# Performance work log

Measured on AMD Instinct MI355X. Metric: run time of the kernel, lower is better.

Reference implementation:

```python
import jax, jax.numpy as jnp
import numpy as np

N, HR, HEADS = 1024, 2048, 4
C1 = HR // HEADS                      # 512 per-head dim, conv1
H2 = 2 * HEADS                        # 8 heads, conv2
C2 = (2 * HR) // (2 * HEADS)          # 512 per-head dim, conv2
EPS = 1e-5


def setup_inputs() -> dict:
    key = jax.random.key(0)
    ks = jax.random.split(key, 20)
    s1 = 1.0 / np.sqrt(N)
    s2 = 1.0 / np.sqrt(HR)
    f32 = jnp.float32
    d = {"x": jax.random.normal(ks[0], (N, N), f32)}
    # conv1 params (in=N, out=HR)
    d["q1_w"] = jax.random.normal(ks[1], (N, HR), f32) * s1
    d["q1_b"] = jnp.zeros((HR,), f32)
    d["k1_w"] = jax.random.normal(ks[2], (N, HR), f32) * s1
    d["k1_b"] = jnp.zeros((HR,), f32)
    d["v1_w"] = jax.random.normal(ks[3], (N, HR), f32) * s1
    d["v1_b"] = jnp.zeros((HR,), f32)
    d["e1_w"] = jax.random.normal(ks[4], (HR,), f32) * 0.1   # lin_edge (edge_dim=1, no bias)
    d["s1_w"] = jax.random.normal(ks[5], (N, HR), f32) * s1  # lin_skip
    d["s1_b"] = jnp.zeros((HR,), f32)
    d["gn1_gamma"] = jnp.ones((HR,), f32)
    d["gn1_beta"] = jnp.zeros((HR,), f32)
    d["gn1_ms"] = jnp.ones((HR,), f32)
    # conv2 params (in=HR, out=2*HR)
    d["q2_w"] = jax.random.normal(ks[6], (HR, 2 * HR), f32) * s2
    d["q2_b"] = jnp.zeros((2 * HR,), f32)
    d["k2_w"] = jax.random.normal(ks[7], (HR, 2 * HR), f32) * s2
    d["k2_b"] = jnp.zeros((2 * HR,), f32)
    d["v2_w"] = jax.random.normal(ks[8], (HR, 2 * HR), f32) * s2
    d["v2_b"] = jnp.zeros((2 * HR,), f32)
    d["e2_w"] = jax.random.normal(ks[9], (2 * HR,), f32) * 0.1
    d["s2_w"] = jax.random.normal(ks[10], (HR, 2 * HR), f32) * s2
    d["s2_b"] = jnp.zeros((2 * HR,), f32)
    d["gn2_gamma"] = jnp.ones((2 * HR,), f32)
    d["gn2_beta"] = jnp.zeros((2 * HR,), f32)
    d["gn2_ms"] = jnp.ones((2 * HR,), f32)
    return d


def _tconv(x, A, qw, qb, kw, kb, vw, vb, ew, sw, sb, H, Cd):
    # TransformerConv over fully-connected meshgrid graph; edge (r -> c) carries scalar A[r, c].
    # key_j/value_j get +A[r,c]*We; the edge term factors out so no [N,N,H,C] tensor is built.
    n = x.shape[0]
    q = (x @ qw + qb).reshape(n, H, Cd)   # targets c
    k = (x @ kw + kb).reshape(n, H, Cd)   # sources r
    v = (x @ vw + vb).reshape(n, H, Cd)
    We = ew.reshape(H, Cd)
    qk = jnp.einsum('chd,rhd->crh', q, k)                 # [N_tgt, N_src, H]
    qe = jnp.einsum('chd,hd->ch', q, We)                  # q_c . We per head
    logits = (qk + A.T[:, :, None] * qe[:, None, :]) / jnp.sqrt(jnp.float32(Cd))
    alpha = jax.nn.softmax(logits, axis=1)                # softmax over sources per target
    out = jnp.einsum('crh,rhd->chd', alpha, v)
    out = out + jnp.einsum('crh,rc->ch', alpha, A)[:, :, None] * We[None]
    return out.reshape(n, H * Cd) + x @ sw + sb           # root/skip connection


def _gnorm(x, gamma, beta, ms):
    # GraphNorm over a single graph: learnable mean-scale, per-feature stats across nodes.
    mu = x.mean(axis=0)
    out = x - ms * mu
    var = (out * out).mean(axis=0)
    return gamma * out * jax.lax.rsqrt(var + EPS) + beta


def reference(x, q1_w, q1_b, k1_w, k1_b, v1_w, v1_b, e1_w, s1_w, s1_b,
              gn1_gamma, gn1_beta, gn1_ms,
              q2_w, q2_b, k2_w, k2_b, v2_w, v2_b, e2_w, s2_w, s2_b,
              gn2_gamma, gn2_beta, gn2_ms):
    A = x  # edge attrs are x.view(-1, 1) over the meshgrid edge_index
    h1 = _tconv(x, A, q1_w, q1_b, k1_w, k1_b, v1_w, v1_b, e1_w, s1_w, s1_b, HEADS, C1)
    h1 = _gnorm(h1, gn1_gamma, gn1_beta, gn1_ms)
    h2 = _tconv(h1, A, q2_w, q2_b, k2_w, k2_b, v2_w, v2_b, e2_w, s2_w, s2_b, H2, C2)
    h2 = _gnorm(h2, gn2_gamma, gn2_beta, gn2_ms)
    return h2 / jnp.linalg.norm(h2, axis=1, keepdims=True)
```

## Files before the change

kernel.cpp:

```cpp
#include <hip/hip_runtime.h>
#include <math.h>

#define EPSV 1e-5f

typedef __attribute__((ext_vector_type(8))) short bf16x8;
typedef __attribute__((ext_vector_type(4))) float f32x4;

__device__ __forceinline__ unsigned short f2bf(float f) {
    unsigned int u = __float_as_uint(f);
    return (unsigned short)((u + 0x7fffu + ((u >> 16) & 1u)) >> 16);
}
__device__ __forceinline__ float b2f(unsigned short u) {
    return __uint_as_float(((unsigned int)u) << 16);
}

__device__ __forceinline__ void glds16(const unsigned short* g, unsigned short* l) {
    __builtin_amdgcn_global_load_lds(
        (const __attribute__((address_space(1))) void*)g,
        (__attribute__((address_space(3))) void*)l, 16, 0, 0);
}

template<int BIAS, int OUTBF>
__global__ __launch_bounds__(256) void gemm_bt(
    const unsigned short* __restrict__ A, const unsigned short* __restrict__ B,
    const float* __restrict__ bias, void* __restrict__ Cout,
    int K, int lda, int ldb, int ldc,
    long aH, long bH, long cH)
{
    __shared__ unsigned short As[4096];
    __shared__ unsigned short Bs[4096];
    const int tid = threadIdx.x;
    const int wid = tid >> 6, lane = tid & 63;
    const int bm = blockIdx.y * 128, bn = blockIdx.x * 128;
    A += (long)blockIdx.z * aH;
    B += (long)blockIdx.z * bH;

    const int wr = wid >> 1, wc = wid & 1;

    const int r0 = (wid << 4) + (lane >> 2);
    const int kq = (lane & 3) << 3;
    const unsigned short* gA0 = A + (long)(bm + r0) * lda + kq;
    const unsigned short* gA1 = gA0 + (long)64 * lda;
    const unsigned short* gB0 = B + (long)(bn + r0) * ldb + kq;
    const unsigned short* gB1 = gB0 + (long)64 * ldb;
    unsigned short* lA0 = &As[wid << 9];
    unsigned short* lA1 = &As[(wid << 9) + 2048];
    unsigned short* lB0 = &Bs[wid << 9];
    unsigned short* lB1 = &Bs[(wid << 9) + 2048];

    f32x4 acc[4][4];
    #pragma unroll
    for (int m = 0; m < 4; m++)
        #pragma unroll
        for (int n = 0; n < 4; n++) acc[m][n] = (f32x4){0.f, 0.f, 0.f, 0.f};

    const int fr = lane & 15;
    const int kb = (lane >> 4) << 3;
    const unsigned short* pA = &As[(wr * 64 + fr) * 32 + kb];
    const unsigned short* pB = &Bs[(wc * 64 + fr) * 32 + kb];

    for (int k0 = 0; k0 < K; k0 += 32) {
        glds16(gA0 + k0, lA0);
        glds16(gA1 + k0, lA1);
        glds16(gB0 + k0, lB0);
        glds16(gB1 + k0, lB1);
        __syncthreads();
        bf16x8 af[4], bfr[4];
        #pragma unroll
        for (int m = 0; m < 4; m++) af[m] = *(const bf16x8*)(pA + (m << 9));
        #pragma unroll
        for (int n = 0; n < 4; n++) bfr[n] = *(const bf16x8*)(pB + (n << 9));
        #pragma unroll
        for (int m = 0; m < 4; m++)
            #pragma unroll
            for (int n = 0; n < 4; n++)
                acc[m][n] = __builtin_amdgcn_mfma_f32_16x16x32_bf16(
                    af[m], bfr[n], acc[m][n], 0, 0, 0);
        __syncthreads();
    }

    const int er = (lane >> 4) << 2;
    const int ec = lane & 15;
    if (OUTBF) {
        unsigned short* C = (unsigned short*)Cout + (long)blockIdx.z * cH;
        #pragma unroll
        for (int m = 0; m < 4; m++)
            #pragma unroll
            for (int n = 0; n < 4; n++) {
                int col = bn + wc * 64 + n * 16 + ec;
                float bv = BIAS ? bias[col] : 0.f;
                #pragma unroll
                for (int j = 0; j < 4; j++) {
                    int row = bm + wr * 64 + m * 16 + er + j;
                    C[(long)row * ldc + col] = f2bf(acc[m][n][j] + bv);
                }
            }
    } else {
        float* C = (float*)Cout + (long)blockIdx.z * cH;
        #pragma unroll
        for (int m = 0; m < 4; m++)
            #pragma unroll
            for (int n = 0; n < 4; n++) {
                int col = bn + wc * 64 + n * 16 + ec;
                #pragma unroll
                for (int j = 0; j < 4; j++) {
                    int row = bm + wr * 64 + m * 16 + er + j;
                    C[(long)row * ldc + col] = acc[m][n][j];
                }
            }
    }
}

__global__ void f2b_kernel(const float* __restrict__ src, unsigned short* __restrict__ dst)
{
    long i = ((long)blockIdx.x * 256 + threadIdx.x) * 8;
    float4 a = *(const float4*)&src[i];
    float4 b = *(const float4*)&src[i + 4];
    unsigned short o[8] = { f2bf(a.x), f2bf(a.y), f2bf(a.z), f2bf(a.w),
                            f2bf(b.x), f2bf(b.y), f2bf(b.z), f2bf(b.w) };
    *(uint4*)&dst[i] = *(uint4*)o;
}

__global__ void transpose_f2b(const float* __restrict__ src, unsigned short* __restrict__ dst,
                              int ldsrc, int Kdim)
{
    __shared__ float t[32][33];
    int f0 = blockIdx.x * 32, k0 = blockIdx.y * 32;
    int tx = threadIdx.x, ty = threadIdx.y;
    #pragma unroll
    for (int i = 0; i < 4; i++)
        t[ty + i * 8][tx] = src[(long)(k0 + ty + i * 8) * ldsrc + f0 + tx];
    __syncthreads();
    #pragma unroll
    for (int i = 0; i < 4; i++)
        dst[(long)(f0 + ty + i * 8) * Kdim + k0 + tx] = f2bf(t[tx][ty + i * 8]);
}

__global__ void transpose_b2b(const unsigned short* __restrict__ src,
                              unsigned short* __restrict__ dst, int ldsrc, int Cd)
{
    __shared__ unsigned short t[32][33];
    int h = blockIdx.z;
    int d0 = blockIdx.x * 32, r0 = blockIdx.y * 32;
    int tx = threadIdx.x, ty = threadIdx.y;
    #pragma unroll
    for (int i = 0; i < 4; i++)
        t[ty + i * 8][tx] = src[(long)(r0 + ty + i * 8) * ldsrc + h * Cd + d0 + tx];
    __syncthreads();
    #pragma unroll
    for (int i = 0; i < 4; i++)
        dst[(long)h * Cd * 1024 + (long)(d0 + ty + i * 8) * 1024 + r0 + tx] = t[tx][ty + i * 8];
}

__global__ void concat4(const float* __restrict__ a, const float* __restrict__ b,
                        const float* __restrict__ c, const float* __restrict__ d,
                        float* __restrict__ o, int F)
{
    int i = blockIdx.x * 256 + threadIdx.x;
    const float* s = (i < F) ? a : (i < 2 * F) ? b : (i < 3 * F) ? c : d;
    o[i] = s[i & (F - 1)];
}

__global__ void transpose1024(const float* __restrict__ in, float* __restrict__ out)
{
    __shared__ float t[32][33];
    int bx = blockIdx.x * 32, by = blockIdx.y * 32;
    #pragma unroll
    for (int i = 0; i < 32; i += 8)
        t[threadIdx.y + i][threadIdx.x] = in[(long)(by + threadIdx.y + i) * 1024 + bx + threadIdx.x];
    __syncthreads();
    #pragma unroll
    for (int i = 0; i < 32; i += 8)
        out[(long)(bx + threadIdx.y + i) * 1024 + by + threadIdx.x] = t[threadIdx.x][threadIdx.y + i];
}

__global__ __launch_bounds__(256) void compute_qe_b(
    const unsigned short* __restrict__ q, const float* __restrict__ ew,
    float* __restrict__ qe, int H, int Cd, int ldq)
{
    int gw = (blockIdx.x * 256 + threadIdx.x) >> 6;
    int lane = threadIdx.x & 63;
    int c = gw / H, h = gw - c * H;
    const unsigned short* qr = q + (long)c * ldq + h * Cd;
    const float* w = ew + h * Cd;
    int d = lane * 8;
    ushort4 u0 = *(const ushort4*)&qr[d];
    ushort4 u1 = *(const ushort4*)&qr[d + 4];
    float4 w0 = *(const float4*)&w[d];
    float4 w1 = *(const float4*)&w[d + 4];
    float s = b2f(u0.x) * w0.x + b2f(u0.y) * w0.y + b2f(u0.z) * w0.z + b2f(u0.w) * w0.w
            + b2f(u1.x) * w1.x + b2f(u1.y) * w1.y + b2f(u1.z) * w1.z + b2f(u1.w) * w1.w;
    #pragma unroll
    for (int o = 32; o; o >>= 1) s += __shfl_xor(s, o);
    if (lane == 0) qe[c * H + h] = s;
}

__global__ __launch_bounds__(256) void softmax_edge(
    const float* __restrict__ S, const float* __restrict__ xT,
    const float* __restrict__ qe, float* __restrict__ aw,
    unsigned short* __restrict__ ab, int H, float inv_sqrt_d)
{
    const int c = blockIdx.x, h = blockIdx.y, tid = threadIdx.x;
    const float* row = S + ((long)h * 1024 + c) * 1024;
    unsigned short* arow = ab + ((long)h * 1024 + c) * 1024;
    const float* xc = xT + (long)c * 1024;
    const float qeh = qe[c * H + h] * inv_sqrt_d;
    float l[4], xv[4];
    float mx = -1e30f;
    #pragma unroll
    for (int i = 0; i < 4; i++) {
        int r = tid + i * 256;
        xv[i] = xc[r];
        l[i] = row[r] * inv_sqrt_d + xv[i] * qeh;
        mx = fmaxf(mx, l[i]);
    }
    __shared__ float red[8];
    #pragma unroll
    for (int o = 32; o; o >>= 1) mx = fmaxf(mx, __shfl_xor(mx, o));
    if ((tid & 63) == 0) red[tid >> 6] = mx;
    __syncthreads();
    mx = fmaxf(fmaxf(red[0], red[1]), fmaxf(red[2], red[3]));
    __syncthreads();
    float e[4], se = 0.f, sa = 0.f;
    #pragma unroll
    for (int i = 0; i < 4; i++) {
        e[i] = __expf(l[i] - mx);
        se += e[i];
        sa += e[i] * xv[i];
    }
    #pragma unroll
    for (int o = 32; o; o >>= 1) { se += __shfl_xor(se, o); sa += __shfl_xor(sa, o); }
    if ((tid & 63) == 0) { red[tid >> 6] = se; red[4 + (tid >> 6)] = sa; }
    __syncthreads();
    se = red[0] + red[1] + red[2] + red[3];
    sa = red[4] + red[5] + red[6] + red[7];
    float inv = 1.f / se;
    #pragma unroll
    for (int i = 0; i < 4; i++) arow[tid + i * 256] = f2bf(e[i] * inv);
    if (tid == 0) aw[c * H + h] = sa * inv;
}

__global__ void combine2(float* __restrict__ out, const unsigned short* __restrict__ skipb,
                         int ldskip, const float* __restrict__ aw, const float* __restrict__ ew,
                         int F, int H)
{
    long idx = ((long)blockIdx.x * 256 + threadIdx.x) * 4;
    int c = (int)(idx / F), f = (int)(idx % F);
    int h = f >> 9;
    float a = aw[c * H + h];
    ushort4 sk = *(const ushort4*)&skipb[(long)c * ldskip + f];
    float4 o = *(float4*)&out[idx];
    float4 w = *(const float4*)&ew[f];
    o.x += b2f(sk.x) + a * w.x; o.y += b2f(sk.y) + a * w.y;
    o.z += b2f(sk.z) + a * w.z; o.w += b2f(sk.w) + a * w.w;
    *(float4*)&out[idx] = o;
}

__global__ void col_stats1(const float* __restrict__ X, float* __restrict__ ps,
                           float* __restrict__ ps2, int F)
{
    int f = blockIdx.x * 256 + threadIdx.x;
    int r0 = blockIdx.y * 32;
    float s = 0.f, s2 = 0.f;
    for (int r = r0; r < r0 + 32; r++) {
        float v = X[(long)r * F + f];
        s += v; s2 += v * v;
    }
    ps [(long)blockIdx.y * F + f] = s;
    ps2[(long)blockIdx.y * F + f] = s2;
}

__global__ void col_stats2(const float* __restrict__ ps, const float* __restrict__ ps2,
    const float* __restrict__ ms, float* __restrict__ msmu, float* __restrict__ rs, int F)
{
    int f = blockIdx.x * 256 + threadIdx.x;
    float s = 0.f, s2 = 0.f;
    for (int ch = 0; ch < 32; ch++) { s += ps[(long)ch * F + f]; s2 += ps2[(long)ch * F + f]; }
    float m  = s  * (1.f / 1024.f);
    float m2 = s2 * (1.f / 1024.f);
    float a = ms[f] * m;
    msmu[f] = a;
    float var = m2 - 2.f * a * m + a * a;
    rs[f] = rsqrtf(var + EPSV);
}

__global__ void gnorm_apply(float* __restrict__ X, const float* __restrict__ msmu,
    const float* __restrict__ rs, const float* __restrict__ g, const float* __restrict__ b, int F)
{
    long idx = ((long)blockIdx.x * 256 + threadIdx.x) * 4;
    int f = (int)(idx % F);
    float4 v = *(float4*)&X[idx];
    v.x = g[f+0] * (v.x - msmu[f+0]) * rs[f+0] + b[f+0];
    v.y = g[f+1] * (v.y - msmu[f+1]) * rs[f+1] + b[f+1];
    v.z = g[f+2] * (v.z - msmu[f+2]) * rs[f+2] + b[f+2];
    v.w = g[f+3] * (v.w - msmu[f+3]) * rs[f+3] + b[f+3];
    *(float4*)&X[idx] = v;
}

__global__ __launch_bounds__(256) void l2norm_rows(float* __restrict__ X, int F)
{
    const int r = blockIdx.x, tid = threadIdx.x;
    float* row = X + (long)r * F;
    float s = 0.f;
    for (int f = tid * 4; f < F; f += 1024) {
        float4 v = *(const float4*)&row[f];
        s += v.x*v.x + v.y*v.y + v.z*v.z + v.w*v.w;
    }
    __shared__ float red[4];
    #pragma unroll
    for (int o = 32; o; o >>= 1) s += __shfl_xor(s, o);
    if ((tid & 63) == 0) red[tid >> 6] = s;
    __syncthreads();
    s = red[0] + red[1] + red[2] + red[3];
    float inv = rsqrtf(s);
    for (int f = tid * 4; f < F; f += 1024) {
        float4 v = *(const float4*)&row[f];
        v.x *= inv; v.y *= inv; v.z *= inv; v.w *= inv;
        *(float4*)&row[f] = v;
    }
}

typedef unsigned short u16;

static inline void launch_gemm(hipStream_t st, const u16* A, const u16* B, const float* bias,
                               void* C, int M, int N, int K, int lda, int ldb, int ldc,
                               int nz, long aH, long bH, long cH, bool outbf)
{
    dim3 g(N / 128, M / 128, nz), b(256);
    if (outbf) {
        if (bias) gemm_bt<1,1><<<g, b, 0, st>>>(A, B, bias, C, K, lda, ldb, ldc, aH, bH, cH);
        else      gemm_bt<0,1><<<g, b, 0, st>>>(A, B, bias, C, K, lda, ldb, ldc, aH, bH, cH);
    } else {
        gemm_bt<0,0><<<g, b, 0, st>>>(A, B, bias, C, K, lda, ldb, ldc, aH, bH, cH);
    }
}

extern "C" void kernel_launch(void* const* d_in, const int* in_sizes, int n_in,
                              void* d_out, int out_size, void* d_ws, size_t ws_size,
                              hipStream_t stream)
{
    const float* x    = (const float*)d_in[0];
    const float* q1w  = (const float*)d_in[1];  const float* q1b = (const float*)d_in[2];
    const float* k1w  = (const float*)d_in[3];  const float* k1b = (const float*)d_in[4];
    const float* v1w  = (const float*)d_in[5];  const float* v1b = (const float*)d_in[6];
    const float* e1w  = (const float*)d_in[7];
    const float* s1w  = (const float*)d_in[8];  const float* s1b = (const float*)d_in[9];
    const float* gn1g = (const float*)d_in[10]; const float* gn1b = (const float*)d_in[11];
    const float* gn1ms= (const float*)d_in[12];
    const float* q2w  = (const float*)d_in[13]; const float* q2b = (const float*)d_in[14];
    const float* k2w  = (const float*)d_in[15]; const float* k2b = (const float*)d_in[16];
    const float* v2w  = (const float*)d_in[17]; const float* v2b = (const float*)d_in[18];
    const float* e2w  = (const float*)d_in[19];
    const float* s2w  = (const float*)d_in[20]; const float* s2b = (const float*)d_in[21];
    const float* gn2g = (const float*)d_in[22]; const float* gn2b = (const float*)d_in[23];
    const float* gn2ms= (const float*)d_in[24];
    float* out = (float*)d_out;

    char* W = (char*)d_ws;
    float* xT    = (float*)W;               W += (long)1024 * 1024 * 4;
    u16*   xb    = (u16*)W;                 W += (long)1024 * 1024 * 2;
    float* h1    = (float*)W;               W += (long)1024 * 2048 * 4;
    u16*   h1b   = (u16*)W;                 W += (long)1024 * 2048 * 2;
    u16*   projC = (u16*)W;                 W += (long)1024 * 16384 * 2;
    char*  R     = W;                       W += (long)8192 * 2048 * 2;
    u16*   WT    = (u16*)R;
    float* S     = (float*)R;
    u16*   ab    = (u16*)W;                 W += (long)8 * 1024 * 1024 * 2;
    u16*   VT    = (u16*)W;                 W += (long)8 * 512 * 1024 * 2;
    float* bc    = (float*)W;               W += 16384 * 4;
    float* qe    = (float*)W;               W += 8192 * 4;
    float* aw    = (float*)W;               W += 8192 * 4;
    float* ps    = (float*)W;               W += (long)32 * 4096 * 4;
    float* ps2   = (float*)W;               W += (long)32 * 4096 * 4;
    float* msmu  = (float*)W;               W += 4096 * 4;
    float* rs    = (float*)W;               W += 4096 * 4;

    const float isd = 1.0f / sqrtf(512.0f);

    transpose1024<<<dim3(32, 32), dim3(32, 8), 0, stream>>>(x, xT);
    f2b_kernel<<<512, 256, 0, stream>>>(x, xb);

    {
        const int F = 2048, K = 1024, H = 4;
        transpose_f2b<<<dim3(64, 32), dim3(32, 8), 0, stream>>>(q1w, WT + (long)0 * F * K, F, K);
        transpose_f2b<<<dim3(64, 32), dim3(32, 8), 0, stream>>>(k1w, WT + (long)1 * F * K, F, K);
        transpose_f2b<<<dim3(64, 32), dim3(32, 8), 0, stream>>>(v1w, WT + (long)2 * F * K, F, K);
        transpose_f2b<<<dim3(64, 32), dim3(32, 8), 0, stream>>>(s1w, WT + (long)3 * F * K, F, K);
        concat4<<<32, 256, 0, stream>>>(q1b, k1b, v1b, s1b, bc, F);
        launch_gemm(stream, xb, WT, bc, projC, 1024, 4 * F, K, K, K, 4 * F, 1, 0, 0, 0, true);

        compute_qe_b<<<1024, 256, 0, stream>>>(projC, e1w, qe, H, 512, 4 * F);
        launch_gemm(stream, projC, projC + F, nullptr, S, 1024, 1024, 512,
                    4 * F, 4 * F, 1024, H, 512, 512, (long)1024 * 1024, false);
        softmax_edge<<<dim3(1024, H), 256, 0, stream>>>(S, xT, qe, aw, ab, H, isd);
        transpose_b2b<<<dim3(16, 32, H), dim3(32, 8), 0, stream>>>(projC + 2 * F, VT, 4 * F, 512);
        launch_gemm(stream, ab, VT, nullptr, h1, 1024, 512, 1024,
                    1024, 1024, F, H, (long)1024 * 1024, (long)512 * 1024, 512, false);
        combine2<<<2048, 256, 0, stream>>>(h1, projC + 3 * F, 4 * F, aw, e1w, F, H);

        col_stats1<<<dim3(F / 256, 32), 256, 0, stream>>>(h1, ps, ps2, F);
        col_stats2<<<F / 256, 256, 0, stream>>>(ps, ps2, gn1ms, msmu, rs, F);
        gnorm_apply<<<(int)((long)1024 * F / 4 / 256), 256, 0, stream>>>(h1, msmu, rs, gn1g, gn1b, F);
    }
    f2b_kernel<<<1024, 256, 0, stream>>>(h1, h1b);

    {
        const int F = 4096, K = 2048, H = 8;
        concat4<<<64, 256, 0, stream>>>(q2b, k2b, v2b, s2b, bc, F);
        transpose_f2b<<<dim3(128, 64), dim3(32, 8), 0, stream>>>(q2w, WT + (long)0 * F * K, F, K);
        transpose_f2b<<<dim3(128, 64), dim3(32, 8), 0, stream>>>(k2w, WT + (long)1 * F * K, F, K);
        launch_gemm(stream, h1b, WT, bc, projC, 1024, 2 * F, K, K, K, 4 * F, 1, 0, 0, 0, true);
        transpose_f2b<<<dim3(128, 64), dim3(32, 8), 0, stream>>>(v2w, WT + (long)0 * F * K, F, K);
        transpose_f2b<<<dim3(128, 64), dim3(32, 8), 0, stream>>>(s2w, WT + (long)1 * F * K, F, K);
        launch_gemm(stream, h1b, WT, bc + 2 * F, projC + 2 * F, 1024, 2 * F, K, K, K, 4 * F, 1, 0, 0, 0, true);

        compute_qe_b<<<2048, 256, 0, stream>>>(projC, e2w, qe, H, 512, 4 * F);
        launch_gemm(stream, projC, projC + F, nullptr, S, 1024, 1024, 512,
                    4 * F, 4 * F, 1024, H, 512, 512, (long)1024 * 1024, false);
        softmax_edge<<<dim3(1024, H), 256, 0, stream>>>(S, xT, qe, aw, ab, H, isd);
        transpose_b2b<<<dim3(16, 32, H), dim3(32, 8), 0, stream>>>(projC + 2 * F, VT, 4 * F, 512);
        launch_gemm(stream, ab, VT, nullptr, out, 1024, 512, 1024,
                    1024, 1024, F, H, (long)1024 * 1024, (long)512 * 1024, 512, false);
        combine2<<<4096, 256, 0, stream>>>(out, projC + 3 * F, 4 * F, aw, e2w, F, H);

        col_stats1<<<dim3(F / 256, 32), 256, 0, stream>>>(out, ps, ps2, F);
        col_stats2<<<F / 256, 256, 0, stream>>>(ps, ps2, gn2ms, msmu, rs, F);
        gnorm_apply<<<(int)((long)1024 * F / 4 / 256), 256, 0, stream>>>(out, msmu, rs, gn2g, gn2b, F);
    }
    l2norm_rows<<<1024, 256, 0, stream>>>(out, 4096);
}
```

Baseline: 585.7 us.

## Add 256-wide pipelined swizzled GEMM, fuse skip/edge epilogue and bf16 gnorm output

Replaces the 128x128 single-buffer GEMM with a 512-thread 128x256 tile kernel. It uses K=64 steps, double-buffered LDS staging, an XOR swizzle and split MFMA phases with setprio to overlap loads with math. The PV GEMM now folds the skip connection and edge term into its epilogue, which removes the combine2 pass. GroupNorm-1 writes bf16 directly, which removes the separate f2b conversion. The new kernel uses much more LDS (96KB) and assumes K is a multiple of 128, which can limit occupancy.

```diff
diff --git a/kernel.cpp b/kernel.cpp
--- a/kernel.cpp
+++ b/kernel.cpp
@@ -5,48 +5,214 @@
 
 typedef __attribute__((ext_vector_type(8))) short bf16x8;
 typedef __attribute__((ext_vector_type(4))) float f32x4;
-
-__device__ __forceinline__ unsigned short f2bf(float f) {
+typedef unsigned short u16;
+
+__device__ __forceinline__ u16 f2bf(float f) {
     unsigned int u = __float_as_uint(f);
-    return (unsigned short)((u + 0x7fffu + ((u >> 16) & 1u)) >> 16);
-}
-__device__ __forceinline__ float b2f(unsigned short u) {
+    return (u16)((u + 0x7fffu + ((u >> 16) & 1u)) >> 16);
+}
+__device__ __forceinline__ float b2f(u16 u) {
     return __uint_as_float(((unsigned int)u) << 16);
 }
 
-__device__ __forceinline__ void glds16(const unsigned short* g, unsigned short* l) {
+__device__ __forceinline__ void glds16(const u16* g, u16* l) {
     __builtin_amdgcn_global_load_lds(
         (const __attribute__((address_space(1))) void*)g,
         (__attribute__((address_space(3))) void*)l, 16, 0, 0);
 }
 
+#define BARRIER() asm volatile("s_barrier" ::: "memory")
+#define VMCNT(n)  asm volatile("s_waitcnt vmcnt(" #n ")" ::: "memory")
+
 template<int BIAS, int OUTBF>
-__global__ __launch_bounds__(256) void gemm_bt(
-    const unsigned short* __restrict__ A, const unsigned short* __restrict__ B,
+__global__ __launch_bounds__(512, 2) void gemm256(
+    const u16* __restrict__ A, const u16* __restrict__ B,
     const float* __restrict__ bias, void* __restrict__ Cout,
-    int K, int lda, int ldb, int ldc,
-    long aH, long bH, long cH)
-{
-    __shared__ unsigned short As[4096];
-    __shared__ unsigned short Bs[4096];
+    int K, int lda, int ldb, int ldc, long aH, long bH, long cH)
+{
+    __shared__ __align__(16) u16 As[16384];
+    __shared__ __align__(16) u16 Bs[32768];
+    const int tid = threadIdx.x;
+    const int wid = tid >> 6, lane = tid & 63;
+    const int wm = wid >> 2, wn = wid & 3;
+    const int fr = lane & 15, g = lane >> 4;
+    const int bm = blockIdx.y * 128, bn = blockIdx.x * 256;
+    A += (long)blockIdx.z * aH;
+    B += (long)blockIdx.z * bH;
+
+    const int srow = tid >> 3;
+    const int kx = ((tid & 7) ^ (srow & 7)) << 3;
+    const u16* gA = A + (long)(bm + srow) * lda + kx;
+    const u16* gB = B + (long)(bn + srow) * ldb + kx;
+    u16* dA = As + (wid << 9);
+    u16* dB = Bs + (wid << 9);
+
+#define STAGE_A(bufi, tt) do { const u16* s_ = gA + (long)(tt) * 64; \
+    u16* d_ = dA + (bufi) * 8192; \
+    glds16(s_, d_); glds16(s_ + 64L * lda, d_ + 4096); } while (0)
+#define STAGE_B01(bufi, tt) do { const u16* s_ = gB + (long)(tt) * 64; \
+    u16* d_ = dB + (bufi) * 16384; \
+    glds16(s_, d_); glds16(s_ + 64L * ldb, d_ + 4096); } while (0)
+#define STAGE_B23(bufi, tt) do { const u16* s_ = gB + (long)(tt) * 64 + 128L * ldb; \
+    u16* d_ = dB + (bufi) * 16384 + 8192; \
+    glds16(s_, d_); glds16(s_ + 64L * ldb, d_ + 4096); } while (0)
+
+    const int q0 = ((0 + g) ^ (fr & 7)) << 3;
+    const int q1 = ((4 + g) ^ (fr & 7)) << 3;
+    const u16* rdA = As + (wm * 64 + fr) * 64;
+    const u16* rdB = Bs + (wn * 64 + fr) * 64;
+
+    bf16x8 am[4][2], bnf[4][2];
+    f32x4 acc[4][4];
+    #pragma unroll
+    for (int m = 0; m < 4; m++)
+        #pragma unroll
+        for (int n = 0; n < 4; n++) acc[m][n] = (f32x4){0.f, 0.f, 0.f, 0.f};
+
+#define RD_AM(bufi) do { const u16* p_ = rdA + (bufi) * 8192; \
+    am[0][0] = *(const bf16x8*)(p_ + q0);        am[0][1] = *(const bf16x8*)(p_ + q1); \
+    am[1][0] = *(const bf16x8*)(p_ + 1024 + q0); am[1][1] = *(const bf16x8*)(p_ + 1024 + q1); \
+    am[2][0] = *(const bf16x8*)(p_ + 2048 + q0); am[2][1] = *(const bf16x8*)(p_ + 2048 + q1); \
+    am[3][0] = *(const bf16x8*)(p_ + 3072 + q0); am[3][1] = *(const bf16x8*)(p_ + 3072 + q1); } while (0)
+#define RD_B01(bufi) do { const u16* p_ = rdB + (bufi) * 16384; \
+    bnf[0][0] = *(const bf16x8*)(p_ + q0);        bnf[0][1] = *(const bf16x8*)(p_ + q1); \
+    bnf[1][0] = *(const bf16x8*)(p_ + 1024 + q0); bnf[1][1] = *(const bf16x8*)(p_ + 1024 + q1); } while (0)
+#define RD_B23(bufi) do { const u16* p_ = rdB + (bufi) * 16384; \
+    bnf[2][0] = *(const bf16x8*)(p_ + 2048 + q0); bnf[2][1] = *(const bf16x8*)(p_ + 2048 + q1); \
+    bnf[3][0] = *(const bf16x8*)(p_ + 3072 + q0); bnf[3][1] = *(const bf16x8*)(p_ + 3072 + q1); } while (0)
+
+#define MFMA_L() do { __builtin_amdgcn_s_setprio(1); \
+    _Pragma("unroll") for (int m_ = 0; m_ < 4; m_++) \
+      _Pragma("unroll") for (int n_ = 0; n_ < 2; n_++) { \
+        acc[m_][n_] = __builtin_amdgcn_mfma_f32_16x16x32_bf16(am[m_][0], bnf[n_][0], acc[m_][n_], 0, 0, 0); \
+        acc[m_][n_] = __builtin_amdgcn_mfma_f32_16x16x32_bf16(am[m_][1], bnf[n_][1], acc[m_][n_], 0, 0, 0); } \
+    __builtin_amdgcn_s_setprio(0); } while (0)
+#define MFMA_R() do { __builtin_amdgcn_s_setprio(1); \
+    _Pragma("unroll") for (int m_ = 0; m_ < 4; m_++) \
+      _Pragma("unroll") for (int n_ = 2; n_ < 4; n_++) { \
+        acc[m_][n_] = __builtin_amdgcn_mfma_f32_16x16x32_bf16(am[m_][0], bnf[n_][0], acc[m_][n_], 0, 0, 0); \
+        acc[m_][n_] = __builtin_amdgcn_mfma_f32_16x16x32_bf16(am[m_][1], bnf[n_][1], acc[m_][n_], 0, 0, 0); } \
+    __builtin_amdgcn_s_setprio(0); } while (0)
+
+    STAGE_A(0, 0); STAGE_B01(0, 0); STAGE_B23(0, 0);
+    STAGE_A(1, 1);
+    VMCNT(2);
+    BARRIER();
+
+    const int NT = K >> 6;
+    const int NITm = (NT >> 1) - 1;
+    for (int it = 0; it < NITm; ++it) {
+        const int t = it << 1;
+        RD_AM(0); RD_B01(0);
+        STAGE_B01(1, t + 1);
+        BARRIER();
+        MFMA_L();
+        BARRIER();
+        RD_B23(0);
+        STAGE_B23(1, t + 1); STAGE_A(0, t + 2);
+        BARRIER();
+        MFMA_R();
+        VMCNT(2);
+        BARRIER();
+        RD_AM(1); RD_B01(1);
+        STAGE_B01(0, t + 2);
+        BARRIER();
+        MFMA_L();
+        BARRIER();
+        RD_B23(1);
+        STAGE_B23(0, t + 2); STAGE_A(1, t + 3);
+        BARRIER();
+        MFMA_R();
+        VMCNT(2);
+        BARRIER();
+    }
+    {
+        const int t = NT - 2;
+        RD_AM(0); RD_B01(0);
+        STAGE_B01(1, t + 1);
+        BARRIER();
+        MFMA_L();
+        BARRIER();
+        RD_B23(0);
+        STAGE_B23(1, t + 1);
+        BARRIER();
+        MFMA_R();
+        VMCNT(0);
+        BARRIER();
+        RD_AM(1); RD_B01(1);
+        BARRIER();
+        MFMA_L();
+        BARRIER();
+        RD_B23(1);
+        BARRIER();
+        MFMA_R();
+    }
+
+    const int er = g << 2;
+    const int crow0 = bm + wm * 64;
+    const int ccol0 = bn + wn * 64;
+    if (OUTBF) {
+        u16* C = (u16*)Cout + (long)blockIdx.z * cH;
+        #pragma unroll
+        for (int m = 0; m < 4; m++)
+            #pragma unroll
+            for (int n = 0; n < 4; n++) {
+                int col = ccol0 + n * 16 + fr;
+                float bv = BIAS ? bias[col] : 0.f;
+                #pragma unroll
+                for (int j = 0; j < 4; j++)
+                    C[(long)(crow0 + m * 16 + er + j) * ldc + col] = f2bf(acc[m][n][j] + bv);
+            }
+    } else {
+        float* C = (float*)Cout + (long)blockIdx.z * cH;
+        #pragma unroll
+        for (int m = 0; m < 4; m++)
+            #pragma unroll
+            for (int n = 0; n < 4; n++) {
+                int col = ccol0 + n * 16 + fr;
+                float bv = BIAS ? bias[col] : 0.f;
+                #pragma unroll
+                for (int j = 0; j < 4; j++)
+                    C[(long)(crow0 + m * 16 + er + j) * ldc + col] = acc[m][n][j] + bv;
+            }
+    }
+#undef STAGE_A
+#undef STAGE_B01
+#undef STAGE_B23
+#undef RD_AM
+#undef RD_B01
+#undef RD_B23
+#undef MFMA_L
+#undef MFMA_R
+}
+
+__global__ __launch_bounds__(256) void gemm_pv(
+    const u16* __restrict__ A, const u16* __restrict__ B,
+    float* __restrict__ C, int K, int lda, int ldb,
+    long aH, long bH,
+    const u16* __restrict__ skipb, int ldsk,
+    const float* __restrict__ aw, const float* __restrict__ ew, int H, int F)
+{
+    __shared__ __align__(16) u16 As[4096];
+    __shared__ __align__(16) u16 Bs[4096];
     const int tid = threadIdx.x;
     const int wid = tid >> 6, lane = tid & 63;
     const int bm = blockIdx.y * 128, bn = blockIdx.x * 128;
-    A += (long)blockIdx.z * aH;
-    B += (long)blockIdx.z * bH;
+    const int h = blockIdx.z;
+    A += (long)h * aH;
+    B += (long)h * bH;
 
     const int wr = wid >> 1, wc = wid & 1;
-
     const int r0 = (wid << 4) + (lane >> 2);
     const int kq = (lane & 3) << 3;
-    const unsigned short* gA0 = A + (long)(bm + r0) * lda + kq;
-    const unsigned short* gA1 = gA0 + (long)64 * lda;
-    const unsigned short* gB0 = B + (long)(bn + r0) * ldb + kq;
-    const unsigned short* gB1 = gB0 + (long)64 * ldb;
-    unsigned short* lA0 = &As[wid << 9];
-    unsigned short* lA1 = &As[(wid << 9) + 2048];
-    unsigned short* lB0 = &Bs[wid << 9];
-    unsigned short* lB1 = &Bs[(wid << 9) + 2048];
+    const u16* gA0 = A + (long)(bm + r0) * lda + kq;
+    const u16* gA1 = gA0 + (long)64 * lda;
+    const u16* gB0 = B + (long)(bn + r0) * ldb + kq;
+    const u16* gB1 = gB0 + (long)64 * ldb;
+    u16* lA0 = &As[wid << 9];
+    u16* lA1 = &As[(wid << 9) + 2048];
+    u16* lB0 = &Bs[wid << 9];
+    u16* lB1 = &Bs[(wid << 9) + 2048];
 
     f32x4 acc[4][4];
     #pragma unroll
@@ -56,8 +222,8 @@
 
     const int fr = lane & 15;
     const int kb = (lane >> 4) << 3;
-    const unsigned short* pA = &As[(wr * 64 + fr) * 32 + kb];
-    const unsigned short* pB = &Bs[(wc * 64 + fr) * 32 + kb];
+    const u16* pA = &As[(wr * 64 + fr) * 32 + kb];
+    const u16* pB = &Bs[(wc * 64 + fr) * 32 + kb];
 
     for (int k0 = 0; k0 < K; k0 += 32) {
         glds16(gA0 + k0, lA0);
@@ -65,63 +231,51 @@
         glds16(gB0 + k0, lB0);
         glds16(gB1 + k0, lB1);
         __syncthreads();
-        bf16x8 af[4], bfr[4];
+        bf16x8 af[4], bf[4];
         #pragma unroll
         for (int m = 0; m < 4; m++) af[m] = *(const bf16x8*)(pA + (m << 9));
         #pragma unroll
-        for (int n = 0; n < 4; n++) bfr[n] = *(const bf16x8*)(pB + (n << 9));
+        for (int n = 0; n < 4; n++) bf[n] = *(const bf16x8*)(pB + (n << 9));
         #pragma unroll
         for (int m = 0; m < 4; m++)
             #pragma unroll
             for (int n = 0; n < 4; n++)
                 acc[m][n] = __builtin_amdgcn_mfma_f32_16x16x32_bf16(
-                    af[m], bfr[n], acc[m][n], 0, 0, 0);
+                    af[m], bf[n], acc[m][n], 0, 0, 0);
         __syncthreads();
     }
 
     const int er = (lane >> 4) << 2;
     const int ec = lane & 15;
-    if (OUTBF) {
-        unsigned short* C = (unsigned short*)Cout + (long)blockIdx.z * cH;
-        #pragma unroll
-        for (int m = 0; m < 4; m++)
+    #pragma unroll
+    for (int m = 0; m < 4; m++)
+        #pragma unroll
+        for (int n = 0; n < 4; n++) {
+            int colh = bn + wc * 64 + n * 16 + ec;
+            int f = h * 512 + colh;
+            float ewf = ew[f];
             #pragma unroll
-            for (int n = 0; n < 4; n++) {
-                int col = bn + wc * 64 + n * 16 + ec;
-                float bv = BIAS ? bias[col] : 0.f;
-                #pragma unroll
-                for (int j = 0; j < 4; j++) {
-                    int row = bm + wr * 64 + m * 16 + er + j;
-                    C[(long)row * ldc + col] = f2bf(acc[m][n][j] + bv);
-                }
+            for (int j = 0; j < 4; j++) {
+                int row = bm + wr * 64 + m * 16 + er + j;
+                float v = acc[m][n][j]
+                        + b2f(skipb[(long)row * ldsk + f])
+                        + aw[row * H + h] * ewf;
+                C[(long)row * F + f] = v;
             }
-    } else {
-        float* C = (float*)Cout + (long)blockIdx.z * cH;
-        #pragma unroll
-        for (int m = 0; m < 4; m++)
-            #pragma unroll
-            for (int n = 0; n < 4; n++) {
-                int col = bn + wc * 64 + n * 16 + ec;
-                #pragma unroll
-                for (int j = 0; j < 4; j++) {
-                    int row = bm + wr * 64 + m * 16 + er + j;
-                    C[(long)row * ldc + col] = acc[m][n][j];
-                }
-            }
-    }
-}
-
-__global__ void f2b_kernel(const float* __restrict__ src, unsigned short* __restrict__ dst)
+        }
+}
+
+__global__ void f2b_kernel(const float* __restrict__ src, u16* __restrict__ dst)
 {
     long i = ((long)blockIdx.x * 256 + threadIdx.x) * 8;
     float4 a = *(const float4*)&src[i];
     float4 b = *(const float4*)&src[i + 4];
-    unsigned short o[8] = { f2bf(a.x), f2bf(a.y), f2bf(a.z), f2bf(a.w),
-                            f2bf(b.x), f2bf(b.y), f2bf(b.z), f2bf(b.w) };
+    u16 o[8] = { f2bf(a.x), f2bf(a.y), f2bf(a.z), f2bf(a.w),
+                 f2bf(b.x), f2bf(b.y), f2bf(b.z), f2bf(b.w) };
     *(uint4*)&dst[i] = *(uint4*)o;
 }
 
-__global__ void transpose_f2b(const float* __restrict__ src, unsigned short* __restrict__ dst,
+__global__ void transpose_f2b(const float* __restrict__ src, u16* __restrict__ dst,
                               int ldsrc, int Kdim)
 {
     __shared__ float t[32][33];
@@ -136,10 +290,10 @@
         dst[(long)(f0 + ty + i * 8) * Kdim + k0 + tx] = f2bf(t[tx][ty + i * 8]);
 }
 
-__global__ void transpose_b2b(const unsigned short* __restrict__ src,
-                              unsigned short* __restrict__ dst, int ldsrc, int Cd)
-{
-    __shared__ unsigned short t[32][33];
+__global__ void transpose_b2b(const u16* __restrict__ src,
+                              u16* __restrict__ dst, int ldsrc, int Cd)
+{
+    __shared__ u16 t[32][33];
     int h = blockIdx.z;
     int d0 = blockIdx.x * 32, r0 = blockIdx.y * 32;
     int tx = threadIdx.x, ty = threadIdx.y;
@@ -175,13 +329,13 @@
 }
 
 __global__ __launch_bounds__(256) void compute_qe_b(
-    const unsigned short* __restrict__ q, const float* __restrict__ ew,
+    const u16* __restrict__ q, const float* __restrict__ ew,
     float* __restrict__ qe, int H, int Cd, int ldq)
 {
     int gw = (blockIdx.x * 256 + threadIdx.x) >> 6;
     int lane = threadIdx.x & 63;
     int c = gw / H, h = gw - c * H;
-    const unsigned short* qr = q + (long)c * ldq + h * Cd;
+    const u16* qr = q + (long)c * ldq + h * Cd;
     const float* w = ew + h * Cd;
     int d = lane * 8;
     ushort4 u0 = *(const ushort4*)&qr[d];
@@ -198,11 +352,11 @@
 __global__ __launch_bounds__(256) void softmax_edge(
     const float* __restrict__ S, const float* __restrict__ xT,
     const float* __restrict__ qe, float* __restrict__ aw,
-    unsigned short* __restrict__ ab, int H, float inv_sqrt_d)
+    u16* __restrict__ ab, int H, float inv_sqrt_d)
 {
     const int c = blockIdx.x, h = blockIdx.y, tid = threadIdx.x;
     const float* row = S + ((long)h * 1024 + c) * 1024;
-    unsigned short* arow = ab + ((long)h * 1024 + c) * 1024;
+    u16* arow = ab + ((long)h * 1024 + c) * 1024;
     const float* xc = xT + (long)c * 1024;
     const float qeh = qe[c * H + h] * inv_sqrt_d;
     float l[4], xv[4];
@@ -238,22 +392,6 @@
     #pragma unroll
     for (int i = 0; i < 4; i++) arow[tid + i * 256] = f2bf(e[i] * inv);
     if (tid == 0) aw[c * H + h] = sa * inv;
-}
-
-__global__ void combine2(float* __restrict__ out, const unsigned short* __restrict__ skipb,
-                         int ldskip, const float* __restrict__ aw, const float* __restrict__ ew,
-                         int F, int H)
-{
-    long idx = ((long)blockIdx.x * 256 + threadIdx.x) * 4;
-    int c = (int)(idx / F), f = (int)(idx % F);
-    int h = f >> 9;
-    float a = aw[c * H + h];
-    ushort4 sk = *(const ushort4*)&skipb[(long)c * ldskip + f];
-    float4 o = *(float4*)&out[idx];
-    float4 w = *(const float4*)&ew[f];
-    o.x += b2f(sk.x) + a * w.x; o.y += b2f(sk.y) + a * w.y;
-    o.z += b2f(sk.z) + a * w.z; o.w += b2f(sk.w) + a * w.w;
-    *(float4*)&out[idx] = o;
 }
 
 __global__ void col_stats1(const float* __restrict__ X, float* __restrict__ ps,
@@ -284,17 +422,25 @@
     rs[f] = rsqrtf(var + EPSV);
 }
 
-__global__ void gnorm_apply(float* __restrict__ X, const float* __restrict__ msmu,
-    const float* __restrict__ rs, const float* __restrict__ g, const float* __restrict__ b, int F)
+template<int OUTBF>
+__global__ void gnorm_apply(const float* __restrict__ X, u16* __restrict__ Yb,
+    float* __restrict__ Yf, const float* __restrict__ msmu,
+    const float* __restrict__ rs, const float* __restrict__ g,
+    const float* __restrict__ b, int F)
 {
     long idx = ((long)blockIdx.x * 256 + threadIdx.x) * 4;
     int f = (int)(idx % F);
-    float4 v = *(float4*)&X[idx];
+    float4 v = *(const float4*)&X[idx];
     v.x = g[f+0] * (v.x - msmu[f+0]) * rs[f+0] + b[f+0];
     v.y = g[f+1] * (v.y - msmu[f+1]) * rs[f+1] + b[f+1];
     v.z = g[f+2] * (v.z - msmu[f+2]) * rs[f+2] + b[f+2];
     v.w = g[f+3] * (v.w - msmu[f+3]) * rs[f+3] + b[f+3];
-    *(float4*)&X[idx] = v;
+    if (OUTBF) {
+        u16 o[4] = { f2bf(v.x), f2bf(v.y), f2bf(v.z), f2bf(v.w) };
+        *(ushort4*)&Yb[idx] = *(ushort4*)o;
+    } else {
+        *(float4*)&Yf[idx] = v;
+    }
 }
 
 __global__ __launch_bounds__(256) void l2norm_rows(float* __restrict__ X, int F)
@@ -320,19 +466,14 @@
     }
 }
 
-typedef unsigned short u16;
-
-static inline void launch_gemm(hipStream_t st, const u16* A, const u16* B, const float* bias,
-                               void* C, int M, int N, int K, int lda, int ldb, int ldc,
-                               int nz, long aH, long bH, long cH, bool outbf)
-{
-    dim3 g(N / 128, M / 128, nz), b(256);
-    if (outbf) {
-        if (bias) gemm_bt<1,1><<<g, b, 0, st>>>(A, B, bias, C, K, lda, ldb, ldc, aH, bH, cH);
-        else      gemm_bt<0,1><<<g, b, 0, st>>>(A, B, bias, C, K, lda, ldb, ldc, aH, bH, cH);
-    } else {
-        gemm_bt<0,0><<<g, b, 0, st>>>(A, B, bias, C, K, lda, ldb, ldc, aH, bH, cH);
-    }
+static inline void launch_g256(hipStream_t st, const u16* A, const u16* B,
+                               const float* bias, void* C, int M, int N, int K,
+                               int lda, int ldb, int ldc, int nz,
+                               long aH, long bH, long cH, bool outbf)
+{
+    dim3 g(N / 256, M / 128, nz), b(512);
+    if (outbf) gemm256<1,1><<<g, b, 0, st>>>(A, B, bias, C, K, lda, ldb, ldc, aH, bH, cH);
+    else       gemm256<0,0><<<g, b, 0, st>>>(A, B, bias, C, K, lda, ldb, ldc, aH, bH, cH);
 }
 
 extern "C" void kernel_launch(void* const* d_in, const int* in_sizes, int n_in,
@@ -387,45 +528,44 @@
         transpose_f2b<<<dim3(64, 32), dim3(32, 8), 0, stream>>>(v1w, WT + (long)2 * F * K, F, K);
         transpose_f2b<<<dim3(64, 32), dim3(32, 8), 0, stream>>>(s1w, WT + (long)3 * F * K, F, K);
         concat4<<<32, 256, 0, stream>>>(q1b, k1b, v1b, s1b, bc, F);
-        launch_gemm(stream, xb, WT, bc, projC, 1024, 4 * F, K, K, K, 4 * F, 1, 0, 0, 0, true);
+        launch_g256(stream, xb, WT, bc, projC, 1024, 4 * F, K, K, K, 4 * F, 1, 0, 0, 0, true);
 
         compute_qe_b<<<1024, 256, 0, stream>>>(projC, e1w, qe, H, 512, 4 * F);
-        launch_gemm(stream, projC, projC + F, nullptr, S, 1024, 1024, 512,
+        launch_g256(stream, projC, projC + F, nullptr, S, 1024, 1024, 512,
                     4 * F, 4 * F, 1024, H, 512, 512, (long)1024 * 1024, false);
         softmax_edge<<<dim3(1024, H), 256, 0, stream>>>(S, xT, qe, aw, ab, H, isd);
         transpose_b2b<<<dim3(16, 32, H), dim3(32, 8), 0, stream>>>(projC + 2 * F, VT, 4 * F, 512);
-        launch_gemm(stream, ab, VT, nullptr, h1, 1024, 512, 1024,
-                    1024, 1024, F, H, (long)1024 * 1024, (long)512 * 1024, 512, false);
-        combine2<<<2048, 256, 0, stream>>>(h1, projC + 3 * F, 4 * F, aw, e1w, F, H);
+        gemm_pv<<<dim3(4, 8, H), 256, 0, stream>>>(ab, VT, h1, 1024, 1024, 1024,
+            (long)1024 * 1024, (long)512 * 1024, projC + 3 * F, 4 * F, aw, e1w, H, F);
 
         col_stats1<<<dim3(F / 256, 32), 256, 0, stream>>>(h1, ps, ps2, F);
         col_stats2<<<F / 256, 256, 0, stream>>>(ps, ps2, gn1ms, msmu, rs, F);
-        gnorm_apply<<<(int)((long)1024 * F / 4 / 256), 256, 0, stream>>>(h1, msmu, rs, gn1g, gn1b, F);
-    }
-    f2b_kernel<<<1024, 256, 0, stream>>>(h1, h1b);
+        gnorm_apply<1><<<(int)((long)1024 * F / 4 / 256), 256, 0, stream>>>(
+            h1, h1b, nullptr, msmu, rs, gn1g, gn1b, F);
+    }
 
     {
         const int F = 4096, K = 2048, H = 8;
         concat4<<<64, 256, 0, stream>>>(q2b, k2b, v2b, s2b, bc, F);
         transpose_f2b<<<dim3(128, 64), dim3(32, 8), 0, stream>>>(q2w, WT + (long)0 * F * K, F, K);
         transpose_f2b<<<dim3(128, 64), dim3(32, 8), 0, stream>>>(k2w, WT + (long)1 * F * K, F, K);
-        launch_gemm(stream, h1b, WT, bc, projC, 1024, 2 * F, K, K, K, 4 * F, 1, 0, 0, 0, true);
+        launch_g256(stream, h1b, WT, bc, projC, 1024, 2 * F, K, K, K, 4 * F, 1, 0, 0, 0, true);
         transpose_f2b<<<dim3(128, 64), dim3(32, 8), 0, stream>>>(v2w, WT + (long)0 * F * K, F, K);
         transpose_f2b<<<dim3(128, 64), dim3(32, 8), 0, stream>>>(s2w, WT + (long)1 * F * K, F, K);
-        launch_gemm(stream, h1b, WT, bc + 2 * F, projC + 2 * F, 1024, 2 * F, K, K, K, 4 * F, 1, 0, 0, 0, true);
+        launch_g256(stream, h1b, WT, bc + 2 * F, projC + 2 * F, 1024, 2 * F, K, K, K, 4 * F, 1, 0, 0, 0, true);
 
         compute_qe_b<<<2048, 256, 0, stream>>>(projC, e2w, qe, H, 512, 4 * F);
-        launch_gemm(stream, projC, projC + F, nullptr, S, 1024, 1024, 512,
+        launch_g256(stream, projC, projC + F, nullptr, S, 1024, 1024, 512,
                     4 * F, 4 * F, 1024, H, 512, 512, (long)1024 * 1024, false);
         softmax_edge<<<dim3(1024, H), 256, 0, stream>>>(S, xT, qe, aw, ab, H, isd);
         transpose_b2b<<<dim3(16, 32, H), dim3(32, 8), 0, stream>>>(projC + 2 * F, VT, 4 * F, 512);
-        launch_gemm(stream, ab, VT, nullptr, out, 1024, 512, 1024,
-                    1024, 1024, F, H, (long)1024 * 1024, (long)512 * 1024, 512, false);
-        combine2<<<4096, 256, 0, stream>>>(out, projC + 3 * F, 4 * F, aw, e2w, F, H);
+        gemm_pv<<<dim3(4, 8, H), 256, 0, stream>>>(ab, VT, out, 1024, 1024, 1024,
+            (long)1024 * 1024, (long)512 * 1024, projC + 3 * F, 4 * F, aw, e2w, H, F);
 
         col_stats1<<<dim3(F / 256, 32), 256, 0, stream>>>(out, ps, ps2, F);
         col_stats2<<<F / 256, 256, 0, stream>>>(ps, ps2, gn2ms, msmu, rs, F);
-        gnorm_apply<<<(int)((long)1024 * F / 4 / 256), 256, 0, stream>>>(out, msmu, rs, gn2g, gn2b, F);
+        gnorm_apply<0><<<(int)((long)1024 * F / 4 / 256), 256, 0, stream>>>(
+            out, nullptr, out, msmu, rs, gn2g, gn2b, F);
     }
     l2norm_rows<<<1024, 256, 0, stream>>>(out, 4096);
 }
```

New measurement: 550.4 us. -6.0%, faster.
